# Optimization experiments

Hardware: AMD Instinct MI355X
Metric: run time of the kernel (lower is better)

The kernel has to match this reference:

```python
import jax, jax.numpy as jnp
import numpy as np

# RWKV6 layer dims (from init_kwargs + fla defaults)
H, DK, DV, NH = 512, 256, 512, 4          # hidden, key_dim, value_dim, heads
HK, HV = DK // NH, DV // NH               # 64, 128
RLOW, WLOW, ID = 32, 64, 1024             # proj_low_rank, decay_low_rank, ffn intermediate
EPS = 1e-5
B, T = 8, 1024


def layernorm(x, g, b):
    m = x.mean(-1, keepdims=True)
    v = ((x - m) ** 2).mean(-1, keepdims=True)
    return (x - m) * jax.lax.rsqrt(v + EPS) * g + b


def token_shift(x):  # shift sequence right by one, zero-pad first token
    return jnp.pad(x, ((0, 0), (1, 0), (0, 0)))[:, :-1]


def rwkv_forward(x, pre_g, pre_b, attn_g, attn_b, ffn_g, ffn_b,
                 xproj_mu, xproj_w1, xproj_w2, x_bias,
                 r_W, w_W1, w_W2, w_b, k_W, v_W, g_W, bonus,
                 gnorm_g, gnorm_b, o_W, fk_mu, fk_W, fv_W, fr_mu, fr_W):
    x0 = layernorm(x, pre_g, pre_b)                 # pre_norm (layer_idx == 0)
    h = layernorm(x0, attn_g, attn_b)               # attn_norm

    # ---- time-mix (RWKV6Attention) ----
    delta = token_shift(h) - h
    # low-rank data-dependent interpolation factors for r,w,k,v,g
    z = jnp.tanh(((h + delta * xproj_mu) @ xproj_w1.T).reshape(B, T, 5, RLOW))
    z = jnp.einsum('blnr,hnr->blnh', z, xproj_w2.reshape(H, 5, RLOW)) + x_bias
    zr, zw, zk, zv, zg = (z[:, :, i] for i in range(5))
    r = ((h + delta * zr) @ r_W.T).reshape(B, T, NH, HK)
    w = jnp.tanh((h + delta * zw) @ w_W1.T) @ w_W2.T + w_b   # decay LoRA
    lw = (-jnp.exp(w)).reshape(B, T, NH, HK)                 # log per-channel decay (< 0)
    k = ((h + delta * zk) @ k_W.T).reshape(B, T, NH, HK)
    v = ((h + delta * zv) @ v_W.T).reshape(B, T, NH, HV)
    g = (h + delta * zg) @ g_W.T

    # WKV6 selective-decay linear recurrence, state S: [B,NH,HK,HV]
    def step(S, inp):
        r_t, k_t, v_t, lw_t = inp
        kv = k_t[..., :, None] * v_t[..., None, :]
        o_t = jnp.einsum('bhk,bhkv->bhv', r_t, S + bonus[None, :, :, None] * kv)
        return jnp.exp(lw_t)[..., None] * S + kv, o_t

    S0 = jnp.zeros((B, NH, HK, HV), x.dtype)
    tfirst = lambda a: jnp.swapaxes(a, 0, 1)
    _, o = jax.lax.scan(step, S0, (tfirst(r), tfirst(k), tfirst(v), tfirst(lw)))
    o = jnp.swapaxes(o, 0, 1)                        # [B,T,NH,HV]

    # GroupNorm(num_heads) over value channels, then swish gate and output proj
    mu = o.mean(-1, keepdims=True)
    var = ((o - mu) ** 2).mean(-1, keepdims=True)
    o = ((o - mu) * jax.lax.rsqrt(var + EPS)).reshape(B, T, DV) * gnorm_g + gnorm_b
    a = (o * (g * jax.nn.sigmoid(g))) @ o_W.T

    res = x0 + a

    # ---- channel-mix (RWKV6FeedForward) ----
    hf = layernorm(res, ffn_g, ffn_b)
    d2 = token_shift(hf) - hf
    kk = jnp.square(jax.nn.relu((hf + d2 * fk_mu) @ fk_W.T))
    val = kk @ fv_W.T
    rec = jax.nn.sigmoid((hf + d2 * fr_mu) @ fr_W.T)
    return res + rec * val


def setup_inputs():
    key = jax.random.key(0)
    ks = iter(jax.random.split(key, 40))
    n = lambda shape, s=0.02: jax.random.normal(next(ks), shape, jnp.float32) * s
    u = lambda shape: jax.random.uniform(next(ks), shape, dtype=jnp.float32)
    return dict(
        x=jax.random.normal(next(ks), (B, T, H), jnp.float32),
        pre_g=jnp.ones(H), pre_b=jnp.zeros(H),
        attn_g=jnp.ones(H), attn_b=jnp.zeros(H),
        ffn_g=jnp.ones(H), ffn_b=jnp.zeros(H),
        xproj_mu=u((H,)), xproj_w1=n((5 * RLOW, H)), xproj_w2=n((H, 5 * RLOW)),
        x_bias=n((5, H)),
        r_W=n((DK, H)),
        w_W1=n((WLOW, H)), w_W2=n((DK, WLOW)), w_b=n((DK,), 0.5),
        k_W=n((DK, H)), v_W=n((DV, H)), g_W=n((DV, H)),
        bonus=n((NH, HK), 0.5),
        gnorm_g=jnp.ones(DV), gnorm_b=jnp.zeros(DV),
        o_W=n((H, DV)),
        fk_mu=u((H,)), fk_W=n((ID, H)),
        fv_W=n((H, ID)),
        fr_mu=u((H,)), fr_W=n((H, H)),
    )


def reference(x, pre_g, pre_b, attn_g, attn_b, ffn_g, ffn_b,
              xproj_mu, xproj_w1, xproj_w2, x_bias,
              r_W, w_W1, w_W2, w_b, k_W, v_W, g_W, bonus,
              gnorm_g, gnorm_b, o_W, fk_mu, fk_W, fv_W, fr_mu, fr_W):
    return rwkv_forward(x, pre_g, pre_b, attn_g, attn_b, ffn_g, ffn_b,
                        xproj_mu, xproj_w1, xproj_w2, x_bias,
                        r_W, w_W1, w_W2, w_b, k_W, v_W, g_W, bonus,
                        gnorm_g, gnorm_b, o_W, fk_mu, fk_W, fv_W, fr_mu, fr_W)
```

## Files before the change

### kernel.cpp

```cpp
#include <hip/hip_runtime.h>


#define DEVINL __device__ __forceinline__

constexpr int B_  = 8, T_ = 1024;
constexpr int BT_ = B_ * T_;
constexpr float EPS_ = 1e-5f;
constexpr int CH_ = 16;
constexpr int NC_ = T_ / CH_;

typedef __bf16 bf16x8 __attribute__((ext_vector_type(8)));
typedef float  f32x4  __attribute__((ext_vector_type(4)));

DEVINL unsigned short f2bs(float f) {
  union { float f; unsigned int i; } c; c.f = f;
  unsigned int x = c.i;
  return (unsigned short)((x + 0x7fffu + ((x >> 16) & 1u)) >> 16);
}
DEVINL float b2f(unsigned short u) {
  union { unsigned int i; float f; } c; c.i = ((unsigned int)u) << 16; return c.f;
}

DEVINL float block_sum256(float v, float* sb) {
  for (int o = 32; o; o >>= 1) v += __shfl_down(v, o);
  int w = threadIdx.x >> 6;
  __syncthreads();
  if ((threadIdx.x & 63) == 0) sb[w] = v;
  __syncthreads();
  return sb[0] + sb[1] + sb[2] + sb[3];
}

DEVINL void gload16(const unsigned short* gsrc, unsigned short* ldsbase) {
  __builtin_amdgcn_global_load_lds(
      (const __attribute__((address_space(1))) unsigned int*)gsrc,
      (__attribute__((address_space(3))) unsigned int*)ldsbase, 16, 0, 0);
}

struct PackSeg { const float* src; int rows, cols, dst_rows; };
struct PackArgs { PackSeg s[12]; int base[13]; };

__global__ __launch_bounds__(256) void pack_kernel(PackArgs pa, unsigned short* dst)
{
  int i = blockIdx.x * 256 + threadIdx.x;
  if (i >= pa.base[12]) return;
  int k = 0;
  while (i >= pa.base[k + 1]) k++;
  int loc = i - pa.base[k];
  PackSeg s = pa.s[k];
  int r = loc / s.cols, c = loc - r * s.cols;
  float v = (r < s.rows) ? s.src[(size_t)r * s.cols + c] : 0.f;
  dst[i] = f2bs(v);
}

__global__ __launch_bounds__(256) void ln2_kernel(
    const float* __restrict__ x,
    const float* __restrict__ pg, const float* __restrict__ pb,
    const float* __restrict__ ag, const float* __restrict__ ab,
    float* __restrict__ x0, unsigned short* __restrict__ h)
{
  __shared__ float sb[4];
  size_t base = (size_t)blockIdx.x * 512;
  int tid = threadIdx.x;
  float v0 = x[base + tid], v1 = x[base + 256 + tid];
  float m = block_sum256(v0 + v1, sb) * (1.f / 512.f);
  float d0 = v0 - m, d1 = v1 - m;
  float var = block_sum256(d0 * d0 + d1 * d1, sb) * (1.f / 512.f);
  float rs = rsqrtf(var + EPS_);
  float a0 = d0 * rs * pg[tid]       + pb[tid];
  float a1 = d1 * rs * pg[tid + 256] + pb[tid + 256];
  x0[base + tid] = a0; x0[base + 256 + tid] = a1;
  float m2 = block_sum256(a0 + a1, sb) * (1.f / 512.f);
  float e0 = a0 - m2, e1 = a1 - m2;
  float var2 = block_sum256(e0 * e0 + e1 * e1, sb) * (1.f / 512.f);
  float rs2 = rsqrtf(var2 + EPS_);
  h[base + tid]       = f2bs(e0 * rs2 * ag[tid]       + ab[tid]);
  h[base + 256 + tid] = f2bs(e1 * rs2 * ag[tid + 256] + ab[tid + 256]);
}

__global__ __launch_bounds__(256) void ln1_kernel(
    const float* __restrict__ in,
    const float* __restrict__ g, const float* __restrict__ b,
    float* __restrict__ out)
{
  __shared__ float sb[4];
  size_t base = (size_t)blockIdx.x * 512;
  int tid = threadIdx.x;
  float v0 = in[base + tid], v1 = in[base + 256 + tid];
  float m = block_sum256(v0 + v1, sb) * (1.f / 512.f);
  float d0 = v0 - m, d1 = v1 - m;
  float var = block_sum256(d0 * d0 + d1 * d1, sb) * (1.f / 512.f);
  float rs = rsqrtf(var + EPS_);
  out[base + tid]       = d0 * rs * g[tid]       + b[tid];
  out[base + 256 + tid] = d1 * rs * g[tid + 256] + b[tid + 256];
}

__global__ __launch_bounds__(256) void ymix_kernel(
    const unsigned short* __restrict__ h, const float* __restrict__ mu,
    unsigned short* __restrict__ y, unsigned short* __restrict__ dl)
{
  int t = blockIdx.x, tid = threadIdx.x, tt = t & (T_ - 1);
  size_t base = (size_t)t * 512;
  for (int c = tid; c < 512; c += 256) {
    float cur  = b2f(h[base + c]);
    float prev = tt ? b2f(h[base - 512 + c]) : 0.f;
    float d = prev - cur;
    dl[base + c] = f2bs(d);
    y[base + c] = f2bs(cur + d * mu[c]);
  }
}

__global__ __launch_bounds__(256) void ffnmix_kernel(
    const float* __restrict__ hf, const float* __restrict__ fkmu,
    const float* __restrict__ frmu,
    unsigned short* __restrict__ mfk, unsigned short* __restrict__ mfr)
{
  int t = blockIdx.x, tid = threadIdx.x, tt = t & (T_ - 1);
  size_t base = (size_t)t * 512;
  for (int c = tid; c < 512; c += 256) {
    float cur  = hf[base + c];
    float prev = tt ? hf[base - 512 + c] : 0.f;
    float d = prev - cur;
    mfk[base + c] = f2bs(cur + d * fkmu[c]);
    mfr[base + c] = f2bs(cur + d * frmu[c]);
  }
}

enum { EP_NONE_F32 = 0, EP_NONE_BF16 = 1, EP_TANH_BF16 = 2, EP_EXPEXP_F32 = 3,
       EP_RES_F32 = 4, EP_RELU2_BF16 = 5, EP_OUT2_F32 = 6, EP_XMIX_BF16 = 7 };

struct GemmDesc {
  const unsigned short* A; const unsigned short* W; void* C;
  const void* bias; const void* aux1; const void* aux2;
  int N, K, lda, ldw, ldc, epi;
};
template <int NG> struct GD { GemmDesc d[NG]; };

template <int BM, int BN, int NG>
__global__ __launch_bounds__(256) void mgemm(GD<NG> p)
{
  GemmDesc dd = p.d[blockIdx.z];
  int n0 = blockIdx.y * BN;
  if (n0 >= dd.N) return;
  int m0 = blockIdx.x * BM;
  constexpr int MFR = BM / 32, NFR = BN / 32;
  constexpr int AIS = BM / 64, WIS = BN / 64;
  constexpr int ASH = (BM == 128) ? 7 : 6;
  constexpr int WSH = (BN == 128) ? 7 : 6;
  __shared__ short As[BM * 32];
  __shared__ short Ws[BN * 32];
  int tid = threadIdx.x, lane = tid & 63, wid = tid >> 6;
  int wm = wid >> 1, wn = wid & 1, lrow = lane & 15, lkg = lane >> 4;

  const unsigned short* aSrc[AIS]; unsigned short* aDst[AIS];
#pragma unroll
  for (int i = 0; i < AIS; i++) {
    int u = i * 256 + wid * 64 + lane;
    int row = u & (BM - 1), kg = u >> ASH;
    aSrc[i] = dd.A + (size_t)(m0 + row) * dd.lda + kg * 8;
    aDst[i] = (unsigned short*)As + (size_t)(i * 256 + wid * 64) * 8;
  }
  const unsigned short* wSrc[WIS]; unsigned short* wDst[WIS];
#pragma unroll
  for (int i = 0; i < WIS; i++) {
    int u = i * 256 + wid * 64 + lane;
    int row = u & (BN - 1), kg = u >> WSH;
    wSrc[i] = dd.W + (size_t)(n0 + row) * dd.ldw + kg * 8;
    wDst[i] = (unsigned short*)Ws + (size_t)(i * 256 + wid * 64) * 8;
  }

  f32x4 acc[MFR][NFR];
#pragma unroll
  for (int mf = 0; mf < MFR; mf++)
#pragma unroll
    for (int nf = 0; nf < NFR; nf++) acc[mf][nf] = (f32x4){0.f, 0.f, 0.f, 0.f};

  for (int kb = 0; kb < dd.K; kb += 32) {
    __syncthreads();
#pragma unroll
    for (int i = 0; i < AIS; i++) gload16(aSrc[i] + kb, aDst[i]);
#pragma unroll
    for (int i = 0; i < WIS; i++) gload16(wSrc[i] + kb, wDst[i]);
    __syncthreads();

    bf16x8 bfrag[NFR];
#pragma unroll
    for (int nf = 0; nf < NFR; nf++)
      bfrag[nf] = *(const bf16x8*)&Ws[((lkg * (BN / 16) + wn * NFR + nf) * 16 + lrow) * 8];
#pragma unroll
    for (int mf = 0; mf < MFR; mf++) {
      bf16x8 afrag = *(const bf16x8*)&As[((lkg * (BM / 16) + wm * MFR + mf) * 16 + lrow) * 8];
#pragma unroll
      for (int nf = 0; nf < NFR; nf++)
        acc[mf][nf] = __builtin_amdgcn_mfma_f32_16x16x32_bf16(
            bfrag[nf], afrag, acc[mf][nf], 0, 0, 0);
    }
  }

#pragma unroll
  for (int mf = 0; mf < MFR; mf++) {
#pragma unroll
    for (int nf = 0; nf < NFR; nf++) {
      int m  = m0 + wm * (MFR * 16) + mf * 16 + lrow;
      int nb = n0 + wn * (NFR * 16) + nf * 16 + lkg * 4;
      size_t off = (size_t)m * dd.ldc + nb;
      float c0 = acc[mf][nf][0], c1 = acc[mf][nf][1];
      float c2 = acc[mf][nf][2], c3 = acc[mf][nf][3];
      switch (dd.epi) {
        case EP_NONE_F32: {
          f32x4 v = {c0, c1, c2, c3};
          *(f32x4*)((float*)dd.C + off) = v; break;
        }
        case EP_NONE_BF16: {
          uint2 u; u.x = f2bs(c0) | ((unsigned)f2bs(c1) << 16);
          u.y = f2bs(c2) | ((unsigned)f2bs(c3) << 16);
          *(uint2*)((unsigned short*)dd.C + off) = u; break;
        }
        case EP_TANH_BF16: {
          uint2 u; u.x = f2bs(tanhf(c0)) | ((unsigned)f2bs(tanhf(c1)) << 16);
          u.y = f2bs(tanhf(c2)) | ((unsigned)f2bs(tanhf(c3)) << 16);
          *(uint2*)((unsigned short*)dd.C + off) = u; break;
        }
        case EP_EXPEXP_F32: {
          const float* bi = (const float*)dd.bias;
          f32x4 v = {expf(-expf(c0 + bi[nb + 0])), expf(-expf(c1 + bi[nb + 1])),
                     expf(-expf(c2 + bi[nb + 2])), expf(-expf(c3 + bi[nb + 3]))};
          *(f32x4*)((float*)dd.C + off) = v; break;
        }
        case EP_RES_F32: {
          f32x4 a = *(const f32x4*)((const float*)dd.aux1 + off);
          f32x4 v = {c0 + a[0], c1 + a[1], c2 + a[2], c3 + a[3]};
          *(f32x4*)((float*)dd.C + off) = v; break;
        }
        case EP_RELU2_BF16: {
          c0 = fmaxf(c0, 0.f); c1 = fmaxf(c1, 0.f);
          c2 = fmaxf(c2, 0.f); c3 = fmaxf(c3, 0.f);
          uint2 u; u.x = f2bs(c0 * c0) | ((unsigned)f2bs(c1 * c1) << 16);
          u.y = f2bs(c2 * c2) | ((unsigned)f2bs(c3 * c3) << 16);
          *(uint2*)((unsigned short*)dd.C + off) = u; break;
        }
        case EP_OUT2_F32: {
          f32x4 rs = *(const f32x4*)((const float*)dd.aux1 + off);
          f32x4 fr = *(const f32x4*)((const float*)dd.aux2 + off);
          f32x4 v = {rs[0] + (1.f / (1.f + expf(-fr[0]))) * c0,
                     rs[1] + (1.f / (1.f + expf(-fr[1]))) * c1,
                     rs[2] + (1.f / (1.f + expf(-fr[2]))) * c2,
                     rs[3] + (1.f / (1.f + expf(-fr[3]))) * c3};
          *(f32x4*)((float*)dd.C + off) = v; break;
        }
        case EP_XMIX_BF16: {
          const float* bi = (const float*)dd.bias;
          uint2 hv = *(const uint2*)((const unsigned short*)dd.aux1 + off);
          uint2 dv = *(const uint2*)((const unsigned short*)dd.aux2 + off);
          const unsigned short* hu = (const unsigned short*)&hv;
          const unsigned short* du = (const unsigned short*)&dv;
          float r0 = b2f(hu[0]) + b2f(du[0]) * (c0 + bi[nb + 0]);
          float r1 = b2f(hu[1]) + b2f(du[1]) * (c1 + bi[nb + 1]);
          float r2 = b2f(hu[2]) + b2f(du[2]) * (c2 + bi[nb + 2]);
          float r3 = b2f(hu[3]) + b2f(du[3]) * (c3 + bi[nb + 3]);
          uint2 u; u.x = f2bs(r0) | ((unsigned)f2bs(r1) << 16);
          u.y = f2bs(r2) | ((unsigned)f2bs(r3) << 16);
          *(uint2*)((unsigned short*)dd.C + off) = u; break;
        }
      }
    }
  }
}

__global__ __launch_bounds__(256) void rbk_kernel(
    const unsigned short* __restrict__ r, const unsigned short* __restrict__ k,
    const float* __restrict__ bonus, float* __restrict__ rbk)
{
  int t = blockIdx.x, tid = threadIdx.x;
  int hh = tid >> 6, j = tid & 63;
  size_t g = (size_t)t * 256 + hh * 64 + j;
  float p = b2f(r[g]) * b2f(k[g]) * bonus[hh * 64 + j];
  for (int o = 32; o; o >>= 1) p += __shfl_down(p, o);
  if (j == 0) rbk[(size_t)t * 4 + hh] = p;
}

__global__ __launch_bounds__(128) void wkv_pass1(
    const unsigned short* __restrict__ k, const float* __restrict__ ew,
    const unsigned short* __restrict__ v, unsigned short* __restrict__ Sl,
    float* __restrict__ Dp)
{
  __shared__ float kL[CH_][64], eL[CH_][64];
  int blk = blockIdx.x;
  int c = blk & (NC_ - 1), bh = blk >> 6;
  int b = bh >> 2, hh = bh & 3;
  int tid = threadIdx.x;
  size_t tbase = (size_t)b * T_ + (size_t)c * CH_;
  for (int idx = tid; idx < CH_ * 64; idx += 128) {
    int s = idx >> 6, j = idx & 63;
    size_t g = (tbase + s) * 256 + hh * 64 + j;
    kL[s][j] = b2f(k[g]); eL[s][j] = ew[g];
  }
  __syncthreads();
  float S[64];
#pragma unroll
  for (int j = 0; j < 64; j++) S[j] = 0.f;
  for (int s = 0; s < CH_; s++) {
    float vv = b2f(v[(tbase + s) * 512 + hh * 128 + tid]);
    const float4* e4p = (const float4*)&eL[s][0];
    const float4* k4p = (const float4*)&kL[s][0];
#pragma unroll
    for (int q = 0; q < 16; q++) {
      float4 e4 = e4p[q], k4 = k4p[q];
      S[4 * q + 0] = e4.x * S[4 * q + 0] + k4.x * vv;
      S[4 * q + 1] = e4.y * S[4 * q + 1] + k4.y * vv;
      S[4 * q + 2] = e4.z * S[4 * q + 2] + k4.z * vv;
      S[4 * q + 3] = e4.w * S[4 * q + 3] + k4.w * vv;
    }
  }
  size_t sbase = (size_t)blk * 8192;
#pragma unroll
  for (int j = 0; j < 64; j++) Sl[sbase + j * 128 + tid] = f2bs(S[j]);
  if (tid < 64) {
    float d = 1.f;
    for (int s = 0; s < CH_; s++) d *= eL[s][tid];
    Dp[(size_t)blk * 64 + tid] = d;
  }
}

__global__ __launch_bounds__(256) void wkv_scan(
    const unsigned short* __restrict__ Sl, const float* __restrict__ Dp,
    unsigned short* __restrict__ Ss)
{
  int e = blockIdx.x * 256 + threadIdx.x;
  int bh = e >> 13; int kv = e & 8191; int j = kv >> 7;
  float run = 0.f;
  for (int c = 0; c < NC_; c++) {
    size_t base = (size_t)bh * NC_ + c;
    Ss[base * 8192 + kv] = f2bs(run);
    run = Dp[base * 64 + j] * run + b2f(Sl[base * 8192 + kv]);
  }
}

__global__ __launch_bounds__(128) void wkv_pass3(
    const unsigned short* __restrict__ r, const unsigned short* __restrict__ k,
    const float* __restrict__ ew, const unsigned short* __restrict__ v,
    const float* __restrict__ rbk, const unsigned short* __restrict__ Ss,
    float* __restrict__ o)
{
  __shared__ float rL[CH_][64], kL[CH_][64], eL[CH_][64], rbL[CH_];
  int blk = blockIdx.x;
  int c = blk & (NC_ - 1), bh = blk >> 6;
  int b = bh >> 2, hh = bh & 3;
  int tid = threadIdx.x;
  size_t tbase = (size_t)b * T_ + (size_t)c * CH_;
  for (int idx = tid; idx < CH_ * 64; idx += 128) {
    int s = idx >> 6, j = idx & 63;
    size_t g = (tbase + s) * 256 + hh * 64 + j;
    rL[s][j] = b2f(r[g]); kL[s][j] = b2f(k[g]); eL[s][j] = ew[g];
  }
  if (tid < CH_) rbL[tid] = rbk[(tbase + tid) * 4 + hh];
  __syncthreads();
  float S[64];
  size_t sbase = (size_t)blk * 8192;
#pragma unroll
  for (int j = 0; j < 64; j++) S[j] = b2f(Ss[sbase + j * 128 + tid]);
  for (int s = 0; s < CH_; s++) {
    float vv = b2f(v[(tbase + s) * 512 + hh * 128 + tid]);
    float oa = rbL[s] * vv;
    const float4* r4p = (const float4*)&rL[s][0];
    const float4* e4p = (const float4*)&eL[s][0];
    const float4* k4p = (const float4*)&kL[s][0];
#pragma unroll
    for (int q = 0; q < 16; q++) {
      float4 r4 = r4p[q], e4 = e4p[q], k4 = k4p[q];
      oa += r4.x * S[4 * q + 0] + r4.y * S[4 * q + 1]
          + r4.z * S[4 * q + 2] + r4.w * S[4 * q + 3];
      S[4 * q + 0] = e4.x * S[4 * q + 0] + k4.x * vv;
      S[4 * q + 1] = e4.y * S[4 * q + 1] + k4.y * vv;
      S[4 * q + 2] = e4.z * S[4 * q + 2] + k4.z * vv;
      S[4 * q + 3] = e4.w * S[4 * q + 3] + k4.w * vv;
    }
    o[(tbase + s) * 512 + hh * 128 + tid] = oa;
  }
}

__global__ __launch_bounds__(256) void gn_gate_kernel(
    const float* __restrict__ o, const unsigned short* __restrict__ g,
    const float* __restrict__ gg, const float* __restrict__ gb,
    unsigned short* __restrict__ obf)
{
  __shared__ float ov[512], ps[64], qs[64], mh[4], vh[4];
  int t = blockIdx.x, tid = threadIdx.x;
  size_t base = (size_t)t * 512;
  ov[tid] = o[base + tid]; ov[tid + 256] = o[base + 256 + tid];
  __syncthreads();
  if (tid < 64) {
    int hh = tid >> 4, sg = tid & 15;
    const float* p = &ov[hh * 128 + sg * 8];
    float s = 0.f, q = 0.f;
    for (int i = 0; i < 8; i++) { s += p[i]; q += p[i] * p[i]; }
    ps[tid] = s; qs[tid] = q;
  }
  __syncthreads();
  if (tid < 4) {
    float s = 0.f, q = 0.f;
    for (int i = 0; i < 16; i++) { s += ps[tid * 16 + i]; q += qs[tid * 16 + i]; }
    float m = s * (1.f / 128.f);
    mh[tid] = m; vh[tid] = q * (1.f / 128.f) - m * m;
  }
  __syncthreads();
  for (int c = tid; c < 512; c += 256) {
    int hh = c >> 7;
    float nrm = (ov[c] - mh[hh]) * rsqrtf(vh[hh] + EPS_);
    float gv = b2f(g[base + c]);
    float sw = gv * (1.f / (1.f + expf(-gv)));
    obf[base + c] = f2bs((nrm * gg[c] + gb[c]) * sw);
  }
}

extern "C" void kernel_launch(void* const* d_in, const int* in_sizes, int n_in,
                              void* d_out, int out_size, void* d_ws, size_t ws_size,
                              hipStream_t stream) {
  (void)in_sizes; (void)n_in; (void)out_size; (void)ws_size;
  const float* x        = (const float*)d_in[0];
  const float* pre_g    = (const float*)d_in[1];
  const float* pre_b    = (const float*)d_in[2];
  const float* attn_g   = (const float*)d_in[3];
  const float* attn_b   = (const float*)d_in[4];
  const float* ffn_g    = (const float*)d_in[5];
  const float* ffn_b    = (const float*)d_in[6];
  const float* xproj_mu = (const float*)d_in[7];
  const float* xproj_w1 = (const float*)d_in[8];
  const float* xproj_w2 = (const float*)d_in[9];
  const float* x_bias   = (const float*)d_in[10];
  const float* r_W      = (const float*)d_in[11];
  const float* w_W1     = (const float*)d_in[12];
  const float* w_W2     = (const float*)d_in[13];
  const float* w_b      = (const float*)d_in[14];
  const float* k_W      = (const float*)d_in[15];
  const float* v_W      = (const float*)d_in[16];
  const float* g_W      = (const float*)d_in[17];
  const float* bonus    = (const float*)d_in[18];
  const float* gnorm_g  = (const float*)d_in[19];
  const float* gnorm_b  = (const float*)d_in[20];
  const float* o_W      = (const float*)d_in[21];
  const float* fk_mu    = (const float*)d_in[22];
  const float* fk_W     = (const float*)d_in[23];
  const float* fv_W     = (const float*)d_in[24];
  const float* fr_mu    = (const float*)d_in[25];
  const float* fr_W     = (const float*)d_in[26];

  const size_t BTH = (size_t)BT_ * 512;
  size_t cur = 0;
  auto alloc = [&](size_t bytes) { void* p = (char*)d_ws + cur; cur += (bytes + 255) & ~(size_t)255; return p; };
  float*          x0    = (float*)alloc(BTH * 4);
  unsigned short* hbufb = (unsigned short*)alloc(BTH * 2);
  unsigned short* m5b   = (unsigned short*)alloc(5 * BTH * 2);
  unsigned short* rbuf  = (unsigned short*)alloc((size_t)BT_ * 256 * 4);
  unsigned short* kbuf  = (unsigned short*)alloc((size_t)BT_ * 256 * 4);
  float*          ebuf  = (float*)alloc((size_t)BT_ * 256 * 4);
  unsigned short* vbuf  = (unsigned short*)alloc(BTH * 4);
  unsigned short* gbuf  = (unsigned short*)alloc(BTH * 4);
  unsigned short* wtmpb = (unsigned short*)alloc((size_t)BT_ * 128 * 2);
  float*          rbk   = (float*)alloc((size_t)BT_ * 4 * 4);
  unsigned short* Sl    = (unsigned short*)alloc((size_t)2048 * 8192 * 2);
  unsigned short* Ss    = (unsigned short*)alloc((size_t)2048 * 8192 * 2);
  float*          Dp    = (float*)alloc((size_t)2048 * 64 * 4);
  float*          res   = (float*)alloc(BTH * 4);
  unsigned short* wpack = (unsigned short*)alloc((size_t)2621440 * 2);
  unsigned short* ybufb = rbuf;
  unsigned short* dlb   = vbuf;
  unsigned short* z5b   = gbuf;
  float*          obuf  = (float*)m5b;
  unsigned short* obf16 = (unsigned short*)ebuf;
  float*          hf    = x0;
  unsigned short* mfk   = rbuf;
  unsigned short* mfr   = kbuf;
  unsigned short* kkb   = Sl;
  float*          frtmp = (float*)vbuf;

  PackArgs pa;
  int off = 0, seg = 0;
  auto addseg = [&](const float* src, int rows, int cols, int dst_rows) {
    pa.s[seg] = {src, rows, cols, dst_rows};
    pa.base[seg] = off; off += dst_rows * cols; seg++;
  };
  addseg(xproj_w1, 160, 512, 192);   int o_w1p = pa.base[0];
  addseg(w_W1,      64, 512, 128);   int o_wW1 = pa.base[1];
  addseg(r_W,      256, 512, 256);   int o_rW  = pa.base[2];
  addseg(k_W,      256, 512, 256);   int o_kW  = pa.base[3];
  addseg(v_W,      512, 512, 512);   int o_vW  = pa.base[4];
  addseg(g_W,      512, 512, 512);   int o_gW  = pa.base[5];
  addseg(o_W,      512, 512, 512);   int o_oW  = pa.base[6];
  addseg(fk_W,    1024, 512, 1024);  int o_fkW = pa.base[7];
  addseg(fv_W,     512, 1024, 512);  int o_fvW = pa.base[8];
  addseg(fr_W,     512, 512, 512);   int o_frW = pa.base[9];
  addseg(w_W2,     256, 64, 256);    int o_wW2 = pa.base[10];
  addseg(xproj_w2, 512, 160, 512);   int o_xw2 = pa.base[11];
  pa.base[12] = off;

  pack_kernel<<<(off + 255) / 256, 256, 0, stream>>>(pa, wpack);
  ln2_kernel<<<BT_, 256, 0, stream>>>(x, pre_g, pre_b, attn_g, attn_b, x0, hbufb);
  ymix_kernel<<<BT_, 256, 0, stream>>>(hbufb, xproj_mu, ybufb, dlb);

  auto solo = [&](const unsigned short* A, const unsigned short* W, void* C,
                  const void* bias, const void* a1, const void* a2,
                  int N, int K, int lda, int ldw, int ldc, int epi) {
    GD<1> g; g.d[0] = {A, W, C, bias, a1, a2, N, K, lda, ldw, ldc, epi};
    mgemm<64, 64, 1><<<dim3(128, (N + 63) / 64, 1), 256, 0, stream>>>(g);
  };

  solo(ybufb, wpack + o_w1p, z5b, nullptr, nullptr, nullptr,
       192, 512, 512, 512, 192, EP_TANH_BF16);

  {
    GD<5> g;
    for (int n = 0; n < 5; n++)
      g.d[n] = {z5b + n * 32, wpack + o_xw2 + n * 32, m5b + (size_t)n * BTH,
                x_bias + n * 512, hbufb, dlb, 512, 32, 192, 160, 512, EP_XMIX_BF16};
    mgemm<128, 128, 5><<<dim3(64, 4, 5), 256, 0, stream>>>(g);
  }

  {
    GD<5> g;
    g.d[0] = {m5b + 0 * BTH, wpack + o_rW, rbuf, nullptr, nullptr, nullptr, 256, 512, 512, 512, 256, EP_NONE_BF16};
    g.d[1] = {m5b + 1 * BTH, wpack + o_wW1, wtmpb, nullptr, nullptr, nullptr, 128, 512, 512, 512, 128, EP_TANH_BF16};
    g.d[2] = {m5b + 2 * BTH, wpack + o_kW, kbuf, nullptr, nullptr, nullptr, 256, 512, 512, 512, 256, EP_NONE_BF16};
    g.d[3] = {m5b + 3 * BTH, wpack + o_vW, vbuf, nullptr, nullptr, nullptr, 512, 512, 512, 512, 512, EP_NONE_BF16};
    g.d[4] = {m5b + 4 * BTH, wpack + o_gW, gbuf, nullptr, nullptr, nullptr, 512, 512, 512, 512, 512, EP_NONE_BF16};
    mgemm<128, 128, 5><<<dim3(64, 4, 5), 256, 0, stream>>>(g);
  }

  solo(wtmpb, wpack + o_wW2, ebuf, w_b, nullptr, nullptr,
       256, 64, 128, 64, 256, EP_EXPEXP_F32);

  rbk_kernel<<<BT_, 256, 0, stream>>>(rbuf, kbuf, bonus, rbk);
  wkv_pass1<<<2048, 128, 0, stream>>>(kbuf, ebuf, vbuf, Sl, Dp);
  wkv_scan<<<1024, 256, 0, stream>>>(Sl, Dp, Ss);
  wkv_pass3<<<2048, 128, 0, stream>>>(rbuf, kbuf, ebuf, vbuf, rbk, Ss, obuf);

  gn_gate_kernel<<<BT_, 256, 0, stream>>>(obuf, gbuf, gnorm_g, gnorm_b, obf16);

  solo(obf16, wpack + o_oW, res, nullptr, x0, nullptr,
       512, 512, 512, 512, 512, EP_RES_F32);

  ln1_kernel<<<BT_, 256, 0, stream>>>(res, ffn_g, ffn_b, hf);
  ffnmix_kernel<<<BT_, 256, 0, stream>>>(hf, fk_mu, fr_mu, mfk, mfr);

  {
    GD<2> g;
    g.d[0] = {mfk, wpack + o_fkW, kkb, nullptr, nullptr, nullptr, 1024, 512, 512, 512, 1024, EP_RELU2_BF16};
    g.d[1] = {mfr, wpack + o_frW, frtmp, nullptr, nullptr, nullptr, 512, 512, 512, 512, 512, EP_NONE_F32};
    mgemm<128, 128, 2><<<dim3(64, 8, 2), 256, 0, stream>>>(g);
  }

  solo(kkb, wpack + o_fvW, (float*)d_out, nullptr, res, frtmp,
       512, 1024, 1024, 1024, 512, EP_OUT2_F32);
}
```

Before: 367.5 us.

## Double-buffer LDS tiles in mgemm to overlap global loads with MFMA

```diff
diff --git a/kernel.cpp b/kernel.cpp
--- a/kernel.cpp
+++ b/kernel.cpp
@@ -144,28 +144,29 @@
   int m0 = blockIdx.x * BM;
   constexpr int MFR = BM / 32, NFR = BN / 32;
   constexpr int AIS = BM / 64, WIS = BN / 64;
+  constexpr int NLD = AIS + WIS;
   constexpr int ASH = (BM == 128) ? 7 : 6;
   constexpr int WSH = (BN == 128) ? 7 : 6;
-  __shared__ short As[BM * 32];
-  __shared__ short Ws[BN * 32];
+  __shared__ unsigned short As[2][BM * 32];
+  __shared__ unsigned short Ws[2][BN * 32];
   int tid = threadIdx.x, lane = tid & 63, wid = tid >> 6;
   int wm = wid >> 1, wn = wid & 1, lrow = lane & 15, lkg = lane >> 4;
 
-  const unsigned short* aSrc[AIS]; unsigned short* aDst[AIS];
+  const unsigned short* aSrc[AIS]; int aOff[AIS];
 #pragma unroll
   for (int i = 0; i < AIS; i++) {
     int u = i * 256 + wid * 64 + lane;
     int row = u & (BM - 1), kg = u >> ASH;
     aSrc[i] = dd.A + (size_t)(m0 + row) * dd.lda + kg * 8;
-    aDst[i] = (unsigned short*)As + (size_t)(i * 256 + wid * 64) * 8;
-  }
-  const unsigned short* wSrc[WIS]; unsigned short* wDst[WIS];
+    aOff[i] = (i * 256 + wid * 64) * 8;
+  }
+  const unsigned short* wSrc[WIS]; int wOff[WIS];
 #pragma unroll
   for (int i = 0; i < WIS; i++) {
     int u = i * 256 + wid * 64 + lane;
     int row = u & (BN - 1), kg = u >> WSH;
     wSrc[i] = dd.W + (size_t)(n0 + row) * dd.ldw + kg * 8;
-    wDst[i] = (unsigned short*)Ws + (size_t)(i * 256 + wid * 64) * 8;
+    wOff[i] = (i * 256 + wid * 64) * 8;
   }
 
   f32x4 acc[MFR][NFR];
@@ -174,26 +175,47 @@
 #pragma unroll
     for (int nf = 0; nf < NFR; nf++) acc[mf][nf] = (f32x4){0.f, 0.f, 0.f, 0.f};
 
-  for (int kb = 0; kb < dd.K; kb += 32) {
-    __syncthreads();
-#pragma unroll
-    for (int i = 0; i < AIS; i++) gload16(aSrc[i] + kb, aDst[i]);
-#pragma unroll
-    for (int i = 0; i < WIS; i++) gload16(wSrc[i] + kb, wDst[i]);
-    __syncthreads();
-
+#pragma unroll
+  for (int i = 0; i < AIS; i++) gload16(aSrc[i], &As[0][0] + aOff[i]);
+#pragma unroll
+  for (int i = 0; i < WIS; i++) gload16(wSrc[i], &Ws[0][0] + wOff[i]);
+
+  int nt = dd.K >> 5;
+  for (int t = 0; t < nt; ++t) {
+    int cb = t & 1;
+    int pbuf = cb ^ 1;
+    if (t + 1 < nt) {
+      int kb2 = (t + 1) << 5;
+      unsigned short* aD = &As[0][0] + pbuf * (BM * 32);
+      unsigned short* wD = &Ws[0][0] + pbuf * (BN * 32);
+#pragma unroll
+      for (int i = 0; i < AIS; i++) gload16(aSrc[i] + kb2, aD + aOff[i]);
+#pragma unroll
+      for (int i = 0; i < WIS; i++) gload16(wSrc[i] + kb2, wD + wOff[i]);
+      if constexpr (NLD == 4) asm volatile("s_waitcnt vmcnt(4)" ::: "memory");
+      else                    asm volatile("s_waitcnt vmcnt(2)" ::: "memory");
+    } else {
+      asm volatile("s_waitcnt vmcnt(0)" ::: "memory");
+    }
+    __builtin_amdgcn_sched_barrier(0);
+    __builtin_amdgcn_s_barrier();
+
+    const unsigned short* AsB = &As[0][0] + cb * (BM * 32);
+    const unsigned short* WsB = &Ws[0][0] + cb * (BN * 32);
     bf16x8 bfrag[NFR];
 #pragma unroll
     for (int nf = 0; nf < NFR; nf++)
-      bfrag[nf] = *(const bf16x8*)&Ws[((lkg * (BN / 16) + wn * NFR + nf) * 16 + lrow) * 8];
+      bfrag[nf] = *(const bf16x8*)&WsB[((lkg * (BN / 16) + wn * NFR + nf) * 16 + lrow) * 8];
 #pragma unroll
     for (int mf = 0; mf < MFR; mf++) {
-      bf16x8 afrag = *(const bf16x8*)&As[((lkg * (BM / 16) + wm * MFR + mf) * 16 + lrow) * 8];
+      bf16x8 afrag = *(const bf16x8*)&AsB[((lkg * (BM / 16) + wm * MFR + mf) * 16 + lrow) * 8];
 #pragma unroll
       for (int nf = 0; nf < NFR; nf++)
         acc[mf][nf] = __builtin_amdgcn_mfma_f32_16x16x32_bf16(
             bfrag[nf], afrag, acc[mf][nf], 0, 0, 0);
     }
+    __builtin_amdgcn_sched_barrier(0);
+    __builtin_amdgcn_s_barrier();
   }
 
 #pragma unroll
```

After: 369.2 us. About the same (+0.5%).
